# Kernel optimization log

Measured on AMD Instinct MI355X. Metric: run time of the kernel, lower is better.

## Reference

```python
import jax, jax.numpy as jnp
import numpy as np

BLOCK_SIZE = 32
QMAX = 31.0   # 6-bit symmetric: representable range [-32, 31], scale by absmax/31
QMIN = -32.0


def axs6_dequant(w: jnp.ndarray, block_size: int = BLOCK_SIZE) -> jnp.ndarray:
    """Block-wise 6-bit symmetric fake-quantization (quantize + dequantize)."""
    shape = w.shape
    wf = w.reshape(-1, block_size)                       # [n_blocks, block]
    scale = jnp.max(jnp.abs(wf), axis=1, keepdims=True) / QMAX
    scale = jnp.where(scale == 0, jnp.ones_like(scale), scale)
    q = jnp.clip(jnp.round(wf / scale), QMIN, QMAX)
    return (q * scale).reshape(shape)


def setup_inputs() -> dict:
    key = jax.random.key(0)
    k_x, k_w, k_b = jax.random.split(key, 3)
    C_in, C_out, K = 256, 512, 3
    x = jax.random.normal(k_x, (32, C_in, 56, 56), dtype=jnp.float32)
    # kaiming_uniform_(a=sqrt(5)) -> bound = sqrt(6 / ((1 + 5) * fan_in)) = 1/sqrt(fan_in)
    fan_in = C_in * K * K
    bound = 1.0 / np.sqrt(fan_in)
    weight = jax.random.uniform(k_w, (C_out, C_in, K, K), dtype=jnp.float32,
                                minval=-bound, maxval=bound)
    bias = jax.random.uniform(k_b, (C_out,), dtype=jnp.float32,
                              minval=-bound, maxval=bound)
    return {"x": x, "weight": weight, "bias": bias}


def reference(x, weight, bias):
    w_dq = axs6_dequant(weight, BLOCK_SIZE)
    out = jax.lax.conv_general_dilated(
        x, w_dq,
        window_strides=(1, 1),
        padding=((1, 1), (1, 1)),
        rhs_dilation=(1, 1),
        feature_group_count=1,
        dimension_numbers=("NCHW", "OIHW", "NCHW"),
    )
    return out + bias[None, :, None, None]
```

## Files before the change

kernel.cpp:

```cpp
#include <hip/hip_runtime.h>
#include <hip/hip_bf16.h>

typedef __bf16 bf16_t;
typedef __attribute__((ext_vector_type(8))) __bf16 bf16x8;
typedef __attribute__((ext_vector_type(4))) float f32x4;
typedef __attribute__((ext_vector_type(4))) int   i32x4;

#define C_IN   256
#define C_OUT  512
#define HW     3136
#define NB     32
#define HP     58
#define NQBLK  36864

#define NT   36
#define NWG  896

typedef const __attribute__((address_space(1))) unsigned int gu32;
typedef __attribute__((address_space(3))) unsigned int lu32;
__device__ __forceinline__ void gl16(const void* g, void* l) {
    __builtin_amdgcn_global_load_lds((gu32*)g, (lu32*)l, 16, 0, 0);
}
#define BAR()    __builtin_amdgcn_s_barrier()
#define PRIO(x)  __builtin_amdgcn_s_setprio(x)
#define SCHED0() __builtin_amdgcn_sched_barrier(0)

__device__ __forceinline__ bf16x8 asbf(i32x4 v) {
    union { i32x4 a; bf16x8 b; } u; u.a = v; return u.b;
}
__device__ __forceinline__ f32x4 MF(i32x4 a, i32x4 b, f32x4 c) {
    return __builtin_amdgcn_mfma_f32_16x16x32_bf16(asbf(a), asbf(b), c, 0, 0, 0);
}

__global__ void k_dequant(const float* __restrict__ w, bf16_t* __restrict__ wt) {
    int b = blockIdx.x * blockDim.x + threadIdx.x;
    if (b >= NQBLK) return;
    const float* src = w + (size_t)b * 32;
    float v[32];
    float amax = 0.f;
    #pragma unroll
    for (int i = 0; i < 32; i += 4) {
        float4 t = *reinterpret_cast<const float4*>(src + i);
        v[i] = t.x; v[i+1] = t.y; v[i+2] = t.z; v[i+3] = t.w;
        amax = fmaxf(amax, fmaxf(fmaxf(fabsf(t.x), fabsf(t.y)),
                                 fmaxf(fabsf(t.z), fabsf(t.w))));
    }
    float scale = amax / 31.0f;
    if (scale == 0.f) scale = 1.f;
    #pragma unroll
    for (int i = 0; i < 32; i++) {
        float q = rintf(v[i] / scale);
        q = fminf(31.f, fmaxf(-32.f, q));
        float dq = q * scale;
        int flat = b * 32 + i;
        int p    = flat % 9;
        int rest = flat / 9;
        int ci   = rest & 255;
        int co   = rest >> 8;
        wt[((size_t)(p * C_OUT + co) << 8) + ci] = (bf16_t)dq;
    }
}

__global__ void k_halo_zero(bf16_t* __restrict__ xT) {
    int idx = blockIdx.x * 256 + threadIdx.x;
    if (idx >= NB * 228 * 32) return;
    int c8 = idx & 31;
    int t  = idx >> 5;
    int p  = t % 228;
    int n  = t / 228;
    int hh, ww;
    if      (p < 58)  { hh = 0;           ww = p; }
    else if (p < 116) { hh = 57;          ww = p - 58; }
    else if (p < 172) { hh = p - 116 + 1; ww = 0; }
    else              { hh = p - 172 + 1; ww = 57; }
    size_t e = (((size_t)n * HP + hh) * HP + ww) * C_IN + c8 * 8;
    *reinterpret_cast<uint4*>(xT + e) = make_uint4(0, 0, 0, 0);
}

__global__ void k_x_nhwc(const float* __restrict__ x, bf16_t* __restrict__ xT) {
    __shared__ float tile[64][65];
    const int n   = blockIdx.z;
    const int cb  = blockIdx.y * 64;
    const int hwb = blockIdx.x * 64;
    const int t   = threadIdx.x;

    const int col = t & 63;
    const int r0  = t >> 6;
    #pragma unroll
    for (int k = 0; k < 16; k++) {
        int r = r0 * 16 + k;
        tile[r][col] = x[((size_t)(n * C_IN + cb + r)) * HW + hwb + col];
    }
    __syncthreads();

    const int j  = t >> 2;
    const int co = (t & 3) * 16;
    const int hw = hwb + j;
    const int hh = hw / 56, ww = hw - hh * 56;
    __align__(16) bf16_t vals[16];
    #pragma unroll
    for (int k = 0; k < 16; k++)
        vals[k] = (bf16_t)tile[co + k][j];
    bf16_t* dst = xT + (((size_t)n * HP + hh + 1) * HP + (ww + 1)) * C_IN + cb + co;
    *reinterpret_cast<uint4*>(dst)     = *reinterpret_cast<uint4*>(&vals[0]);
    *reinterpret_cast<uint4*>(dst + 8) = *reinterpret_cast<uint4*>(&vals[8]);
}

__global__ __launch_bounds__(512, 2) void k_conv_gemm(
    const bf16_t* __restrict__ xT, const bf16_t* __restrict__ wt,
    const float* __restrict__ bias, float* __restrict__ out)
{
    __shared__ __align__(16) bf16_t As[3][256][64];
    __shared__ __align__(16) bf16_t Bs[2][224][64];

    const int tid  = threadIdx.x;
    const int lane = tid & 63;
    const int wid  = tid >> 6;
    const int wr   = wid >> 1;
    const int wc   = wid & 1;

    const int orig  = blockIdx.x;
    const int wgid  = (orig & 7) * 112 + (orig >> 3);
    const int co0   = (wgid & 1) * 256;
    const int sband = wgid >> 1;
    const int nimg  = sband / 14;
    const int R0    = (sband - nimg * 14) * 4;

    const int trow = tid >> 3;
    const int lcx  = (tid & 7) ^ (trow & 7);

    const bf16_t* pA[4];
    const bf16_t* pB[4];
    #pragma unroll
    for (int i = 0; i < 4; i++) {
        pA[i] = wt + ((size_t)(co0 + i * 64 + trow) << 8) + lcx * 8;
        int r  = i * 64 + trow;
        int br = r / 56, bc = r - br * 56;
        pB[i] = xT + (((size_t)nimg * HP + R0 + br + 1) * HP + (bc + 1)) * C_IN + lcx * 8;
    }

    auto stageA2 = [&](int slot, int tk, int part) {
        const size_t off = ((size_t)(tk >> 2) << 17) + ((tk & 3) << 6);
        bf16_t* dst = &As[slot][0][0] + wid * 512;
        if (part == 0) { gl16(pA[0] + off, dst);        gl16(pA[1] + off, dst + 4096); }
        else           { gl16(pA[2] + off, dst + 8192); gl16(pA[3] + off, dst + 12288); }
    };
    auto stageB2 = [&](int buf, int tk, int part) {
        const int p  = tk >> 2;
        const int q3 = p / 3;
        const int off = ((q3 - 1) * HP + (p - q3 * 3) - 1) * C_IN + ((tk & 3) << 6);
        bf16_t* dst = &Bs[buf][0][0] + wid * 512;
        if (part == 0) { gl16(pB[0] + off, dst);        gl16(pB[1] + off, dst + 4096); }
        else           { gl16(pB[2] + off, dst + 8192);
                         if (tid < 256) gl16(pB[3] + off, dst + 12288); }
    };

    const int rl = lane & 15;
    const int kg = lane >> 4;
    const unsigned asBase = (unsigned)(uintptr_t)&As[0][0][0];
    const unsigned bsBase = (unsigned)(uintptr_t)&Bs[0][0][0];
    const unsigned aAddr0 = asBase + (unsigned)((wr * 64 + rl) * 128 + ((kg       ^ (rl & 7)) * 16));
    const unsigned aAddr1 = asBase + (unsigned)((wr * 64 + rl) * 128 + (((4 + kg) ^ (rl & 7)) * 16));
    const unsigned bAddr0 = bsBase + (unsigned)((wc * 112 + rl) * 128 + ((kg       ^ (rl & 7)) * 16));
    const unsigned bAddr1 = bsBase + (unsigned)((wc * 112 + rl) * 128 + (((4 + kg) ^ (rl & 7)) * 16));

    f32x4 acc[4][7];
    #pragma unroll
    for (int m = 0; m < 4; m++)
        #pragma unroll
        for (int j = 0; j < 7; j++)
            acc[m][j] = f32x4{0.f, 0.f, 0.f, 0.f};

#define RD2(D0, D1, A0, A1, OFFS) \
    asm volatile("ds_read_b128 %0, %2 offset:" OFFS "\n\t" \
                 "ds_read_b128 %1, %3 offset:" OFFS \
                 : "=v"(D0), "=v"(D1) : "v"(A0), "v"(A1));
#define LGKM(N) asm volatile("s_waitcnt lgkmcnt(" N ")" ::: "memory"); SCHED0();
#define MFMA8(AA, J, X0, X1) \
    PRIO(1); \
    acc[0][J] = MF(AA##00, X0, acc[0][J]); acc[0][J] = MF(AA##01, X1, acc[0][J]); \
    acc[1][J] = MF(AA##10, X0, acc[1][J]); acc[1][J] = MF(AA##11, X1, acc[1][J]); \
    acc[2][J] = MF(AA##20, X0, acc[2][J]); acc[2][J] = MF(AA##21, X1, acc[2][J]); \
    acc[3][J] = MF(AA##30, X0, acc[3][J]); acc[3][J] = MF(AA##31, X1, acc[3][J]); \
    PRIO(0);

#define TILE(AC, AN, T, SR1, SR2, BCUR) do {                                  \
    const unsigned bT0 = bAddr0 + (unsigned)(BCUR) * 28672u;                  \
    const unsigned bT1 = bAddr1 + (unsigned)(BCUR) * 28672u;                  \
    const unsigned nT0 = aAddr0 + (unsigned)(SR1) * 32768u;                   \
    const unsigned nT1 = aAddr1 + (unsigned)(SR1) * 32768u;                   \
    RD2(S00, S01, bT0, bT1, "0");                                             \
    RD2(S10, S11, bT0, bT1, "2048");                                          \
                                                                      \
    RD2(S20, S21, bT0, bT1, "4096");                                          \
    if ((T) + 2 < NT) stageA2((SR2), (T) + 2, 0);                             \
    LGKM("4");  MFMA8(AC, 0, S00, S01);                                       \
                                                                      \
    RD2(S00, S01, bT0, bT1, "6144");                                          \
    RD2(AN##00, AN##01, nT0, nT1, "0");                                       \
    if ((T) + 2 < NT) stageA2((SR2), (T) + 2, 1);                             \
    LGKM("6");  MFMA8(AC, 1, S10, S11);                                       \
                                                                      \
    RD2(S10, S11, bT0, bT1, "8192");                                          \
    RD2(AN##10, AN##11, nT0, nT1, "2048");                                    \
    if ((T) + 1 < NT) stageB2(((T) + 1) & 1, (T) + 1, 0);                     \
    LGKM("8");  MFMA8(AC, 2, S20, S21);                                       \
                                                                      \
    RD2(S20, S21, bT0, bT1, "10240");                                         \
    RD2(AN##20, AN##21, nT0, nT1, "4096");                                    \
    if ((T) + 1 < NT) stageB2(((T) + 1) & 1, (T) + 1, 1);                     \
    LGKM("10"); MFMA8(AC, 3, S00, S01);                                       \
                                                                      \
    RD2(S00, S01, bT0, bT1, "12288");                                         \
    RD2(AN##30, AN##31, nT0, nT1, "6144");                                    \
    LGKM("10"); MFMA8(AC, 4, S10, S11);                                       \
                                                                      \
    LGKM("6");  MFMA8(AC, 5, S20, S21);                                       \
                                                                      \
    LGKM("2");  MFMA8(AC, 6, S00, S01);                                       \
    asm volatile("s_waitcnt vmcnt(0)" ::: "memory");                          \
    BAR();                                                                    \
    SCHED0();                                                                 \
} while (0)

    i32x4 Ea00, Ea01, Ea10, Ea11, Ea20, Ea21, Ea30, Ea31;
    i32x4 Eb00, Eb01, Eb10, Eb11, Eb20, Eb21, Eb30, Eb31;
    i32x4 S00, S01, S10, S11, S20, S21;

    stageA2(0, 0, 0); stageA2(0, 0, 1);
    stageA2(1, 1, 0); stageA2(1, 1, 1);
    stageB2(0, 0, 0); stageB2(0, 0, 1);
    asm volatile("s_waitcnt vmcnt(0)" ::: "memory");
    BAR();
    SCHED0();
    RD2(Ea00, Ea01, aAddr0, aAddr1, "0");
    RD2(Ea10, Ea11, aAddr0, aAddr1, "2048");
    RD2(Ea20, Ea21, aAddr0, aAddr1, "4096");
    RD2(Ea30, Ea31, aAddr0, aAddr1, "6144");

    int sr = 0;
    #pragma unroll 1
    for (int t = 0; t < NT; t += 2) {
        const int sr1 = (sr + 1 >= 3) ? sr - 2 : sr + 1;
        const int sr2 = (sr + 2 >= 3) ? sr - 1 : sr + 2;
        TILE(Ea, Eb, t,     sr1, sr2, 0);
        TILE(Eb, Ea, t + 1, sr2, sr,  1);
        sr = sr2;
    }
    asm volatile("s_waitcnt lgkmcnt(0)" ::: "memory");
    SCHED0();

#undef RD2
#undef LGKM
#undef MFMA8
#undef TILE

    int hw_off[7];
    #pragma unroll
    for (int j = 0; j < 7; j++) {
        int nn = wc * 112 + j * 16 + rl;
        int br = nn / 56, bc = nn - br * 56;
        hw_off[j] = (R0 + br) * 56 + bc;
    }
    const size_t obase = (size_t)nimg * C_OUT * HW;
    #pragma unroll
    for (int m = 0; m < 4; m++) {
        int cob = co0 + wr * 64 + m * 16 + ((lane >> 4) << 2);
        #pragma unroll
        for (int i = 0; i < 4; i++) {
            int co = cob + i;
            float bv = bias[co];
            float* orow = out + obase + (size_t)co * HW;
            #pragma unroll
            for (int j = 0; j < 7; j++)
                orow[hw_off[j]] = acc[m][j][i] + bv;
        }
    }
}

extern "C" void kernel_launch(void* const* d_in, const int* in_sizes, int n_in,
                              void* d_out, int out_size, void* d_ws, size_t ws_size,
                              hipStream_t stream) {
    const float* x    = (const float*)d_in[0];
    const float* w    = (const float*)d_in[1];
    const float* bias = (const float*)d_in[2];
    float* out = (float*)d_out;

    bf16_t* xT = (bf16_t*)d_ws;
    bf16_t* wt = (bf16_t*)((char*)d_ws + (size_t)NB * HP * HP * C_IN * 2);

    k_halo_zero<<<dim3((NB * 228 * 32 + 255) / 256), dim3(256), 0, stream>>>(xT);
    k_x_nhwc<<<dim3(49, 4, NB), dim3(256), 0, stream>>>(x, xT);
    k_dequant<<<dim3((NQBLK + 255) / 256), dim3(256), 0, stream>>>(w, wt);
    k_conv_gemm<<<dim3(NWG), dim3(512), 0, stream>>>(xT, wt, bias, out);
}
```

Before: 260.7 us.

## Triple-buffer B tiles, double-buffer A, and prefetch next B fragments across barrier

Swaps the LDS buffering so A uses two stages and B uses three. The loop is unrolled by six to cycle B stages, and B prefetch is issued two tiles ahead. The first two B fragments of the next tile are read before the barrier. The wait before the barrier is relaxed to vmcnt(4), so loads for tile T+2 stay in flight across it. This aims to hide global-load and LDS-read latency at tile boundaries, at the cost of more live registers and more complex stage indexing. LDS footprint changes slightly (B stage is smaller than A).

```diff
diff --git a/kernel.cpp b/kernel.cpp
--- a/kernel.cpp
+++ b/kernel.cpp
@@ -110,8 +110,8 @@
     const bf16_t* __restrict__ xT, const bf16_t* __restrict__ wt,
     const float* __restrict__ bias, float* __restrict__ out)
 {
-    __shared__ __align__(16) bf16_t As[3][256][64];
-    __shared__ __align__(16) bf16_t Bs[2][224][64];
+    __shared__ __align__(16) bf16_t As[2][256][64];
+    __shared__ __align__(16) bf16_t Bs[3][224][64];
 
     const int tid  = threadIdx.x;
     const int lane = tid & 63;
@@ -184,41 +184,46 @@
     acc[3][J] = MF(AA##30, X0, acc[3][J]); acc[3][J] = MF(AA##31, X1, acc[3][J]); \
     PRIO(0);
 
-#define TILE(AC, AN, T, SR1, SR2, BCUR) do {                                  \
-    const unsigned bT0 = bAddr0 + (unsigned)(BCUR) * 28672u;                  \
-    const unsigned bT1 = bAddr1 + (unsigned)(BCUR) * 28672u;                  \
-    const unsigned nT0 = aAddr0 + (unsigned)(SR1) * 32768u;                   \
-    const unsigned nT1 = aAddr1 + (unsigned)(SR1) * 32768u;                   \
-    RD2(S00, S01, bT0, bT1, "0");                                             \
-    RD2(S10, S11, bT0, bT1, "2048");                                          \
-                                                                      \
-    RD2(S20, S21, bT0, bT1, "4096");                                          \
-    if ((T) + 2 < NT) stageA2((SR2), (T) + 2, 0);                             \
-    LGKM("4");  MFMA8(AC, 0, S00, S01);                                       \
-                                                                      \
-    RD2(S00, S01, bT0, bT1, "6144");                                          \
-    RD2(AN##00, AN##01, nT0, nT1, "0");                                       \
-    if ((T) + 2 < NT) stageA2((SR2), (T) + 2, 1);                             \
-    LGKM("6");  MFMA8(AC, 1, S10, S11);                                       \
-                                                                      \
-    RD2(S10, S11, bT0, bT1, "8192");                                          \
-    RD2(AN##10, AN##11, nT0, nT1, "2048");                                    \
-    if ((T) + 1 < NT) stageB2(((T) + 1) & 1, (T) + 1, 0);                     \
-    LGKM("8");  MFMA8(AC, 2, S20, S21);                                       \
-                                                                      \
-    RD2(S20, S21, bT0, bT1, "10240");                                         \
-    RD2(AN##20, AN##21, nT0, nT1, "4096");                                    \
-    if ((T) + 1 < NT) stageB2(((T) + 1) & 1, (T) + 1, 1);                     \
-    LGKM("10"); MFMA8(AC, 3, S00, S01);                                       \
-                                                                      \
-    RD2(S00, S01, bT0, bT1, "12288");                                         \
-    RD2(AN##30, AN##31, nT0, nT1, "6144");                                    \
-    LGKM("10"); MFMA8(AC, 4, S10, S11);                                       \
-                                                                      \
-    LGKM("6");  MFMA8(AC, 5, S20, S21);                                       \
-                                                                      \
-    LGKM("2");  MFMA8(AC, 6, S00, S01);                                       \
-    asm volatile("s_waitcnt vmcnt(0)" ::: "memory");                          \
+#define TILE(AC, AN, T, BC, BNX, BST) do {                                    \
+    const unsigned bT0 = bAddr0 + (unsigned)(BC) * 28672u;                    \
+    const unsigned bT1 = bAddr1 + (unsigned)(BC) * 28672u;                    \
+    const unsigned nA0 = aAddr0 + (unsigned)(((T) + 1) & 1) * 32768u;         \
+    const unsigned nA1 = aAddr1 + (unsigned)(((T) + 1) & 1) * 32768u;         \
+    const unsigned pT0 = bAddr0 + (unsigned)(BNX) * 28672u;                   \
+    const unsigned pT1 = bAddr1 + (unsigned)(BNX) * 28672u;                   \
+                                                                      \
+    RD2(S00, S01, bT0, bT1, "4096");                                          \
+    if ((T) + 2 < NT) stageA2((T) & 1, (T) + 2, 0);                           \
+    LGKM("4");  MFMA8(AC, 0, T00, T01);                                       \
+                                                                      \
+    RD2(S10, S11, bT0, bT1, "6144");                                          \
+    RD2(AN##00, AN##01, nA0, nA1, "0");                                       \
+    if ((T) + 2 < NT) stageA2((T) & 1, (T) + 2, 1);                           \
+    LGKM("6");  MFMA8(AC, 1, T10, T11);                                       \
+                                                                      \
+    RD2(S20, S21, bT0, bT1, "8192");                                          \
+    RD2(AN##10, AN##11, nA0, nA1, "2048");                                    \
+    if ((T) + 2 < NT) stageB2((BST), (T) + 2, 0);                             \
+    LGKM("8");  MFMA8(AC, 2, S00, S01);                                       \
+                                                                      \
+    RD2(S00, S01, bT0, bT1, "10240");                                         \
+    RD2(AN##20, AN##21, nA0, nA1, "4096");                                    \
+    if ((T) + 2 < NT) stageB2((BST), (T) + 2, 1);                             \
+    LGKM("10"); MFMA8(AC, 3, S10, S11);                                       \
+                                                                      \
+    RD2(S10, S11, bT0, bT1, "12288");                                         \
+    RD2(AN##30, AN##31, nA0, nA1, "6144");                                    \
+    LGKM("10"); MFMA8(AC, 4, S20, S21);                                       \
+                                                    \
+    RD2(T00, T01, pT0, pT1, "0");                                             \
+    LGKM("8");  MFMA8(AC, 5, S00, S01);                                       \
+                                                    \
+    RD2(T10, T11, pT0, pT1, "2048");                                          \
+    LGKM("6");  MFMA8(AC, 6, S10, S11);                                       \
+    if ((T) + 2 < NT)                                                         \
+        asm volatile("s_waitcnt vmcnt(4)" ::: "memory");                      \
+    else                                                                      \
+        asm volatile("s_waitcnt vmcnt(0)" ::: "memory");                      \
     BAR();                                                                    \
     SCHED0();                                                                 \
 } while (0)
@@ -226,10 +231,12 @@
     i32x4 Ea00, Ea01, Ea10, Ea11, Ea20, Ea21, Ea30, Ea31;
     i32x4 Eb00, Eb01, Eb10, Eb11, Eb20, Eb21, Eb30, Eb31;
     i32x4 S00, S01, S10, S11, S20, S21;
+    i32x4 T00, T01, T10, T11;
 
     stageA2(0, 0, 0); stageA2(0, 0, 1);
     stageA2(1, 1, 0); stageA2(1, 1, 1);
     stageB2(0, 0, 0); stageB2(0, 0, 1);
+    stageB2(1, 1, 0); stageB2(1, 1, 1);
     asm volatile("s_waitcnt vmcnt(0)" ::: "memory");
     BAR();
     SCHED0();
@@ -237,15 +244,18 @@
     RD2(Ea10, Ea11, aAddr0, aAddr1, "2048");
     RD2(Ea20, Ea21, aAddr0, aAddr1, "4096");
     RD2(Ea30, Ea31, aAddr0, aAddr1, "6144");
-
-    int sr = 0;
+    RD2(T00, T01, bAddr0, bAddr1, "0");
+    RD2(T10, T11, bAddr0, bAddr1, "2048");
+    LGKM("6");
+
     #pragma unroll 1
-    for (int t = 0; t < NT; t += 2) {
-        const int sr1 = (sr + 1 >= 3) ? sr - 2 : sr + 1;
-        const int sr2 = (sr + 2 >= 3) ? sr - 1 : sr + 2;
-        TILE(Ea, Eb, t,     sr1, sr2, 0);
-        TILE(Eb, Ea, t + 1, sr2, sr,  1);
-        sr = sr2;
+    for (int t = 0; t < NT; t += 6) {
+        TILE(Ea, Eb, t + 0, 0, 1, 2);
+        TILE(Eb, Ea, t + 1, 1, 2, 0);
+        TILE(Ea, Eb, t + 2, 2, 0, 1);
+        TILE(Eb, Ea, t + 3, 0, 1, 2);
+        TILE(Ea, Eb, t + 4, 1, 2, 0);
+        TILE(Eb, Ea, t + 5, 2, 0, 1);
     }
     asm volatile("s_waitcnt lgkmcnt(0)" ::: "memory");
     SCHED0();
```

Result: slower. 342.3 us (+31.3%).
